# Kernel tuning notes

Measured on AMD Instinct MI355X. Metric: run time of the kernel, lower is better.

## Reference

```python
import jax, jax.numpy as jnp
import numpy as np

DEGREE = 4
NUM_CHARTS = 8
N = 16384
IN_DIM = 29  # 3*(2*4+1) + 2 procedural params


def positional_encoding(x, degree=DEGREE):
    # Faithful to torch order: [x, sin(2^1 pi x), cos(2^1 pi x), ..., sin(2^d pi x), cos(2^d pi x)]
    pe = [x]
    for d in range(1, degree + 1):
        s = (2.0 ** d) * np.pi
        pe.append(jnp.sin(s * x))
        pe.append(jnp.cos(s * x))
    return jnp.concatenate(pe, axis=-1)


def setup_inputs() -> dict:
    key = jax.random.key(0)
    ks = jax.random.split(key, 9)
    h = 256
    sc = 0.05
    return {
        "x": jax.random.normal(ks[0], (N, 3), jnp.float32),
        "proc": jax.random.normal(ks[1], (1, 2), jnp.float32),
        "W0": jax.random.normal(ks[2], (NUM_CHARTS, IN_DIM, h), jnp.float32) * sc,
        "b0": jax.random.normal(ks[3], (NUM_CHARTS, h), jnp.float32) * sc,
        "Wh": jax.random.normal(ks[4], (NUM_CHARTS, 6, h, h), jnp.float32) * sc,
        "bh": jax.random.normal(ks[5], (NUM_CHARTS, 6, h), jnp.float32) * sc,
        "Wl": jax.random.normal(ks[6], (NUM_CHARTS, h, 2), jnp.float32) * sc,
        "bl": jax.random.normal(ks[7], (NUM_CHARTS, 2), jnp.float32) * sc,
        "mlp_idx": jax.random.randint(ks[8], (N,), 0, NUM_CHARTS, jnp.int32),
    }


def reference(x, proc, W0, b0, Wh, bh, Wl, bl, mlp_idx):
    xp = positional_encoding(x)                      # (N, 27)
    proc_rep = jnp.broadcast_to(proc, (xp.shape[0], proc.shape[1]))
    xp = jnp.concatenate([xp, proc_rep], axis=-1)    # (N, 29)

    out = jnp.zeros((xp.shape[0], Wl.shape[-1]), xp.dtype)
    n_hidden = Wh.shape[1]
    for c in range(NUM_CHARTS):                      # small fixed chart loop
        h = jax.nn.relu(xp @ W0[c] + b0[c])          # (N, 256)
        for l in range(n_hidden):
            h = jax.nn.relu(h @ Wh[c, l] + bh[c, l])
        oc = jax.nn.sigmoid(h @ Wl[c] + bl[c])       # (N, 2)
        out = jnp.where((mlp_idx == c)[:, None], oc, out)
    return out
```

## Files before the change

kernel.cpp:

```cpp
#include <hip/hip_runtime.h>
#include <hip/hip_bf16.h>
#include <math.h>

#define NPTS   16384
#define NCH    8
#define MT     32
#define LSTR   264
#define SEG    16384
#define PSEG   2048

typedef short bf16x8 __attribute__((ext_vector_type(8)));
typedef float f32x4  __attribute__((ext_vector_type(4)));

__device__ __forceinline__ float bf2f(unsigned short u){
  union { unsigned int i; float f; } v; v.i = ((unsigned int)u) << 16; return v.f;
}
__device__ __forceinline__ unsigned short f2bf(float f){
  union { float f; unsigned int i; } v; v.f = f;
  unsigned int x = v.i;
  return (unsigned short)((x + 0x7fffu + ((x >> 16) & 1u)) >> 16);
}


__global__ __launch_bounds__(256) void prep_k(
    const float* __restrict__ Wh, const float* __restrict__ W0,
    const int* __restrict__ midx,
    unsigned short* __restrict__ Wth, unsigned short* __restrict__ Wt0,
    int* __restrict__ segcnt, int* __restrict__ bucket){
  int bid = blockIdx.x, tid = threadIdx.x;
  if (bid < 192){
    __shared__ __align__(16) unsigned short tile[64 * LSTR];
    int mat = bid >> 2, ck = bid & 3;
    const float* src = Wh + (size_t)mat * 65536 + (size_t)ck * 64 * 256;
    int r = tid >> 2, seg = (tid & 3) * 64;
    const float* sp = &src[r * 256 + seg];
    #pragma unroll
    for (int j8 = 0; j8 < 8; j8++){
      float4 f0 = *(const float4*)&sp[j8 * 8];
      float4 f1 = *(const float4*)&sp[j8 * 8 + 4];
      __align__(16) unsigned short t8[8];
      t8[0]=f2bf(f0.x); t8[1]=f2bf(f0.y); t8[2]=f2bf(f0.z); t8[3]=f2bf(f0.w);
      t8[4]=f2bf(f1.x); t8[5]=f2bf(f1.y); t8[6]=f2bf(f1.z); t8[7]=f2bf(f1.w);
      *(uint4*)&tile[r * LSTR + seg + j8 * 8] = *(const uint4*)t8;
    }
    __syncthreads();
    unsigned short* dst = Wth + (size_t)mat * 65536 + (size_t)ck * 16384;
    #pragma unroll
    for (int it = 0; it < 8; it++){
      int s = it * 256 + tid;
      int k8l = s >> 8, n = s & 255;
      __align__(16) unsigned short t8[8];
      #pragma unroll
      for (int j = 0; j < 8; j++) t8[j] = tile[(k8l * 8 + j) * LSTR + n];
      *(uint4*)&dst[(size_t)s * 8] = *(const uint4*)t8;
    }
  } else if (bid < 200){
    int c = bid - 192;
    #pragma unroll
    for (int it = 0; it < 4; it++){
      int s = it * 256 + tid;
      int k8 = s >> 8, n = s & 255;
      __align__(16) unsigned short t8[8];
      #pragma unroll
      for (int j = 0; j < 8; j++){
        int k = k8 * 8 + j;
        t8[j] = (k < 29) ? f2bf(W0[(c * 29 + k) * 256 + n]) : (unsigned short)0;
      }
      *(uint4*)&Wt0[(size_t)c * 8192 + (size_t)s * 8] = *(const uint4*)t8;
    }
  } else {
    __shared__ int cur[NCH];
    int sb = bid - 200;
    int lane = tid & 63;
    if (tid < NCH) cur[tid] = 0;
    __syncthreads();
    for (int it = 0; it < 8; it++){
      int i = sb * PSEG + it * 256 + tid;
      int c = midx[i];
      #pragma unroll
      for (int cc = 0; cc < NCH; cc++){
        unsigned long long m = __ballot(c == cc);
        if (!m) continue;
        int leader = (int)(__ffsll((long long)m) - 1);
        int wb = 0;
        if (lane == leader) wb = atomicAdd(&cur[cc], (int)__popcll(m));
        wb = __shfl(wb, leader);
        if (c == cc){
          int rk = (int)__popcll(m & ((1ull << lane) - 1));
          bucket[cc * SEG + sb * PSEG + wb + rk] = i;
        }
      }
    }
    __syncthreads();
    if (tid < NCH) segcnt[sb * NCH + tid] = cur[tid];
  }
}


#define LOADG(g) do {                                                          \
    const unsigned short* _p = wlane + (size_t)(g) * 8192;                     \
    asm volatile("global_load_dwordx4 %0, %4, off\n\t"                         \
                 "global_load_dwordx4 %1, %4, off offset:256\n\t"              \
                 "global_load_dwordx4 %2, %4, off offset:512\n\t"              \
                 "global_load_dwordx4 %3, %4, off offset:768"                  \
        : "=&v"(br[g][0]), "=&v"(br[g][1]), "=&v"(br[g][2]), "=&v"(br[g][3])   \
        : "v"(_p));                                                            \
  } while (0)

#define WAITG(g, n)                                                            \
  asm volatile("s_waitcnt vmcnt(" #n ")"                                       \
      : "+v"(br[g][0]), "+v"(br[g][1]), "+v"(br[g][2]), "+v"(br[g][3]))

#define MFMAG(g)                                                               \
  {                                                                            \
    bf16x8 a0 = *(const bf16x8*)&ain[(l15) * LSTR + (g) * 32 + quad * 8];      \
    bf16x8 a1 = *(const bf16x8*)&ain[(16 + l15) * LSTR + (g) * 32 + quad * 8]; \
    _Pragma("unroll")                                                          \
    for (int nt = 0; nt < 4; nt++){                                            \
      acc[0][nt] = __builtin_amdgcn_mfma_f32_16x16x32_bf16(                    \
          a0, br[g][nt], ((g) == 0) ? zz : acc[0][nt], 0, 0, 0);               \
      acc[1][nt] = __builtin_amdgcn_mfma_f32_16x16x32_bf16(                    \
          a1, br[g][nt], ((g) == 0) ? zz : acc[1][nt], 0, 0, 0);               \
    }                                                                          \
  }

__global__ __launch_bounds__(256) void mlp_k(
    const float* __restrict__ x,
    const float* __restrict__ proc,
    const float* __restrict__ b0,
    const float* __restrict__ bh,
    const float* __restrict__ Wl,
    const float* __restrict__ bl,
    const unsigned short* __restrict__ Wt0,
    const unsigned short* __restrict__ Wth,
    const int* __restrict__ segcnt,
    const int* __restrict__ bucket,
    float* __restrict__ out)
{
  __shared__ __align__(16) unsigned short actA[MT * LSTR];
  __shared__ __align__(16) unsigned short actB[MT * LSTR];
  __shared__ unsigned short biasb[7 * 256];
  __shared__ unsigned short wlb[512];
  __shared__ int ridx[MT];

  int chart = blockIdx.x & 7;
  int tile  = blockIdx.x >> 3;

  int pre[9];
  pre[0] = 0;
  #pragma unroll
  for (int s = 0; s < 8; s++) pre[s + 1] = pre[s] + segcnt[s * NCH + chart];
  int total = pre[8];
  int cnt = total - tile * MT;
  if (cnt <= 0) return;
  if (cnt > MT) cnt = MT;

  int tid  = threadIdx.x;
  int lane = tid & 63;
  int wv   = tid >> 6;
  int l15  = lane & 15;
  int quad = lane >> 4;
  int cb   = wv * 64;

  biasb[tid] = f2bf(b0[chart * 256 + tid]);
  #pragma unroll
  for (int j = 0; j < 6; j++)
    biasb[(j + 1) * 256 + tid] = f2bf(bh[(chart * 6 + j) * 256 + tid]);
  wlb[tid]       = f2bf(Wl[chart * 512 + tid]);
  wlb[256 + tid] = f2bf(Wl[chart * 512 + 256 + tid]);

  if (tid < MT){
    int row = tid;
    int g = -1;
    if (row < cnt){
      int r = tile * MT + row;
      int sb = 0, off = 0;
      #pragma unroll
      for (int s = 0; s < 8; s++)
        if (r >= pre[s]){ sb = s; off = r - pre[s]; }
      g = bucket[chart * SEG + sb * PSEG + off];
    }
    ridx[row] = g;
    unsigned short* rowp = &actA[row * LSTR];
    if (g >= 0){
      float xv0 = x[g*3+0], xv1 = x[g*3+1], xv2 = x[g*3+2];
      rowp[0] = f2bf(xv0); rowp[1] = f2bf(xv1); rowp[2] = f2bf(xv2);
      #pragma unroll
      for (int d = 1; d <= 4; d++){
        float s = (float)(1 << d) * 3.14159265358979323846f;
        int o = 3 + (d - 1) * 6;
        rowp[o+0] = f2bf(sinf(s*xv0)); rowp[o+1] = f2bf(sinf(s*xv1)); rowp[o+2] = f2bf(sinf(s*xv2));
        rowp[o+3] = f2bf(cosf(s*xv0)); rowp[o+4] = f2bf(cosf(s*xv1)); rowp[o+5] = f2bf(cosf(s*xv2));
      }
      rowp[27] = f2bf(proc[0]); rowp[28] = f2bf(proc[1]);
      rowp[29] = 0; rowp[30] = 0; rowp[31] = 0;
    } else {
      #pragma unroll
      for (int k = 0; k < 32; k++) rowp[k] = 0;
    }
  }
  __syncthreads();

  f32x4 acc[2][4];
  const f32x4 zz = {0.f, 0.f, 0.f, 0.f};

  {
    const unsigned short* W0p = Wt0 + chart * 8192;
    bf16x8 b0r[4];
    #pragma unroll
    for (int nt = 0; nt < 4; nt++)
      b0r[nt] = *(const bf16x8*)&W0p[(size_t)(quad * 256 + cb + nt * 16 + l15) * 8];
    #pragma unroll
    for (int mt = 0; mt < 2; mt++){
      bf16x8 a0 = *(const bf16x8*)&actA[(mt * 16 + l15) * LSTR + quad * 8];
      #pragma unroll
      for (int nt = 0; nt < 4; nt++)
        acc[mt][nt] = __builtin_amdgcn_mfma_f32_16x16x32_bf16(a0, b0r[nt], zz, 0, 0, 0);
    }
    #pragma unroll
    for (int nt = 0; nt < 4; nt++){
      int col = cb + nt * 16 + l15;
      float bias = bf2f(biasb[col]);
      #pragma unroll
      for (int mt = 0; mt < 2; mt++)
        #pragma unroll
        for (int r = 0; r < 4; r++){
          float v = acc[mt][nt][r] + bias;
          v = v > 0.f ? v : 0.f;
          actB[(mt * 16 + quad * 4 + r) * LSTR + col] = f2bf(v);
        }
    }
  }
  __syncthreads();

  for (int l = 1; l <= 6; l++){
    const unsigned short* wlane = Wth + ((size_t)(chart * 6 + l - 1) << 16)
                                + (size_t)(quad * 256 + cb + l15) * 8;
    const unsigned short* ain = (l & 1) ? actB : actA;
    unsigned short* aout      = (l & 1) ? actA : actB;

    bf16x8 br[8][4];
    LOADG(0); LOADG(1); LOADG(2); LOADG(3);
    LOADG(4); LOADG(5); LOADG(6); LOADG(7);

    WAITG(0, 28); MFMAG(0);
    WAITG(1, 24); MFMAG(1);
    WAITG(2, 20); MFMAG(2);
    WAITG(3, 16); MFMAG(3);
    WAITG(4, 12); MFMAG(4);
    WAITG(5, 8);  MFMAG(5);
    WAITG(6, 4);  MFMAG(6);
    WAITG(7, 0);  MFMAG(7);

    #pragma unroll
    for (int nt = 0; nt < 4; nt++){
      int col = cb + nt * 16 + l15;
      float bias = bf2f(biasb[l * 256 + col]);
      #pragma unroll
      for (int mt = 0; mt < 2; mt++)
        #pragma unroll
        for (int r = 0; r < 4; r++){
          float v = acc[mt][nt][r] + bias;
          v = v > 0.f ? v : 0.f;
          aout[(mt * 16 + quad * 4 + r) * LSTR + col] = f2bf(v);
        }
    }
    __syncthreads();
  }

  {
    int m = tid >> 3;
    int p = tid & 7;
    const unsigned short* hrow = actB + m * LSTR + p * 32;
    const unsigned short* wlp = wlb + p * 64;
    float s0 = 0.f, s1 = 0.f;
    #pragma unroll 8
    for (int k = 0; k < 32; k += 2){
      unsigned int w01 = *(const unsigned int*)&wlp[k * 2];
      unsigned int w23 = *(const unsigned int*)&wlp[k * 2 + 2];
      unsigned int h2  = *(const unsigned int*)&hrow[k];
      float hv0 = bf2f((unsigned short)(h2 & 0xffff));
      float hv1 = bf2f((unsigned short)(h2 >> 16));
      s0 += hv0 * bf2f((unsigned short)(w01 & 0xffff)) + hv1 * bf2f((unsigned short)(w23 & 0xffff));
      s1 += hv0 * bf2f((unsigned short)(w01 >> 16))    + hv1 * bf2f((unsigned short)(w23 >> 16));
    }
    s0 += __shfl_xor(s0, 1); s0 += __shfl_xor(s0, 2); s0 += __shfl_xor(s0, 4);
    s1 += __shfl_xor(s1, 1); s1 += __shfl_xor(s1, 2); s1 += __shfl_xor(s1, 4);
    if (p == 0){
      int g = ridx[m];
      if (g >= 0){
        float o0 = 1.f / (1.f + __expf(-(s0 + bl[chart*2+0])));
        float o1 = 1.f / (1.f + __expf(-(s1 + bl[chart*2+1])));
        *(float2*)&out[(size_t)g * 2] = make_float2(o0, o1);
      }
    }
  }
}


extern "C" void kernel_launch(void* const* d_in, const int* in_sizes, int n_in,
                              void* d_out, int out_size, void* d_ws, size_t ws_size,
                              hipStream_t stream){
  const float* x    = (const float*)d_in[0];
  const float* proc = (const float*)d_in[1];
  const float* W0   = (const float*)d_in[2];
  const float* b0   = (const float*)d_in[3];
  const float* Wh   = (const float*)d_in[4];
  const float* bh   = (const float*)d_in[5];
  const float* Wl   = (const float*)d_in[6];
  const float* bl   = (const float*)d_in[7];
  const int* midx = (const int*)d_in[8];
  float* out = (float*)d_out;

  char* ws = (char*)d_ws;
  int* segcnt = (int*)ws;
  int* bucket = segcnt + 64;
  size_t off = (((size_t)(64 + NCH * SEG)) * 4 + 15) & ~(size_t)15;
  unsigned short* Wt0 = (unsigned short*)(ws + off);
  unsigned short* Wth = Wt0 + NCH * 8192;

  hipLaunchKernelGGL(prep_k, dim3(208),  dim3(256), 0, stream,
                     Wh, W0, midx, Wth, Wt0, segcnt, bucket);
  hipLaunchKernelGGL(mlp_k,  dim3(4096), dim3(256), 0, stream,
                     x, proc, b0, bh, Wl, bl, Wt0, Wth, segcnt, bucket, out);
}
```

Baseline: 128.6 us.

## Double MLP row tile to 64 and software-pipeline weight loads with four slots

```diff
diff --git a/kernel.cpp b/kernel.cpp
--- a/kernel.cpp
+++ b/kernel.cpp
@@ -4,7 +4,7 @@
 
 #define NPTS   16384
 #define NCH    8
-#define MT     32
+#define MT     64
 #define LSTR   264
 #define SEG    16384
 #define PSEG   2048
@@ -97,34 +97,35 @@
 }
 
 
-#define LOADG(g) do {                                                          \
+#define LOADG(slot, g) do {                                                    \
     const unsigned short* _p = wlane + (size_t)(g) * 8192;                     \
     asm volatile("global_load_dwordx4 %0, %4, off\n\t"                         \
                  "global_load_dwordx4 %1, %4, off offset:256\n\t"              \
                  "global_load_dwordx4 %2, %4, off offset:512\n\t"              \
                  "global_load_dwordx4 %3, %4, off offset:768"                  \
-        : "=&v"(br[g][0]), "=&v"(br[g][1]), "=&v"(br[g][2]), "=&v"(br[g][3])   \
+        : "=&v"(br[slot][0]), "=&v"(br[slot][1]),                              \
+          "=&v"(br[slot][2]), "=&v"(br[slot][3])                               \
         : "v"(_p));                                                            \
   } while (0)
 
-#define WAITG(g, n)                                                            \
+#define WAITG(slot, n)                                                         \
   asm volatile("s_waitcnt vmcnt(" #n ")"                                       \
-      : "+v"(br[g][0]), "+v"(br[g][1]), "+v"(br[g][2]), "+v"(br[g][3]))
-
-#define MFMAG(g)                                                               \
+      : "+v"(br[slot][0]), "+v"(br[slot][1]),                                  \
+        "+v"(br[slot][2]), "+v"(br[slot][3]))
+
+#define MFMAG(slot, g)                                                         \
   {                                                                            \
-    bf16x8 a0 = *(const bf16x8*)&ain[(l15) * LSTR + (g) * 32 + quad * 8];      \
-    bf16x8 a1 = *(const bf16x8*)&ain[(16 + l15) * LSTR + (g) * 32 + quad * 8]; \
     _Pragma("unroll")                                                          \
-    for (int nt = 0; nt < 4; nt++){                                            \
-      acc[0][nt] = __builtin_amdgcn_mfma_f32_16x16x32_bf16(                    \
-          a0, br[g][nt], ((g) == 0) ? zz : acc[0][nt], 0, 0, 0);               \
-      acc[1][nt] = __builtin_amdgcn_mfma_f32_16x16x32_bf16(                    \
-          a1, br[g][nt], ((g) == 0) ? zz : acc[1][nt], 0, 0, 0);               \
+    for (int mt = 0; mt < 4; mt++){                                            \
+      bf16x8 a = *(const bf16x8*)&ain[(mt * 16 + l15) * LSTR + (g) * 32 + quad * 8]; \
+      _Pragma("unroll")                                                        \
+      for (int nt = 0; nt < 4; nt++)                                           \
+        acc[mt][nt] = __builtin_amdgcn_mfma_f32_16x16x32_bf16(                 \
+            a, br[slot][nt], ((g) == 0) ? zz : acc[mt][nt], 0, 0, 0);          \
     }                                                                          \
   }
 
-__global__ __launch_bounds__(256) void mlp_k(
+__global__ __launch_bounds__(256, 1) void mlp_k(
     const float* __restrict__ x,
     const float* __restrict__ proc,
     const float* __restrict__ b0,
@@ -201,7 +202,7 @@
   }
   __syncthreads();
 
-  f32x4 acc[2][4];
+  f32x4 acc[4][4];
   const f32x4 zz = {0.f, 0.f, 0.f, 0.f};
 
   {
@@ -211,7 +212,7 @@
     for (int nt = 0; nt < 4; nt++)
       b0r[nt] = *(const bf16x8*)&W0p[(size_t)(quad * 256 + cb + nt * 16 + l15) * 8];
     #pragma unroll
-    for (int mt = 0; mt < 2; mt++){
+    for (int mt = 0; mt < 4; mt++){
       bf16x8 a0 = *(const bf16x8*)&actA[(mt * 16 + l15) * LSTR + quad * 8];
       #pragma unroll
       for (int nt = 0; nt < 4; nt++)
@@ -222,7 +223,7 @@
       int col = cb + nt * 16 + l15;
       float bias = bf2f(biasb[col]);
       #pragma unroll
-      for (int mt = 0; mt < 2; mt++)
+      for (int mt = 0; mt < 4; mt++)
         #pragma unroll
         for (int r = 0; r < 4; r++){
           float v = acc[mt][nt][r] + bias;
@@ -239,25 +240,24 @@
     const unsigned short* ain = (l & 1) ? actB : actA;
     unsigned short* aout      = (l & 1) ? actA : actB;
 
-    bf16x8 br[8][4];
-    LOADG(0); LOADG(1); LOADG(2); LOADG(3);
-    LOADG(4); LOADG(5); LOADG(6); LOADG(7);
-
-    WAITG(0, 28); MFMAG(0);
-    WAITG(1, 24); MFMAG(1);
-    WAITG(2, 20); MFMAG(2);
-    WAITG(3, 16); MFMAG(3);
-    WAITG(4, 12); MFMAG(4);
-    WAITG(5, 8);  MFMAG(5);
-    WAITG(6, 4);  MFMAG(6);
-    WAITG(7, 0);  MFMAG(7);
+    bf16x8 br[4][4];
+    LOADG(0, 0); LOADG(1, 1); LOADG(2, 2); LOADG(3, 3);
+
+    WAITG(0, 12); MFMAG(0, 0); LOADG(0, 4);
+    WAITG(1, 12); MFMAG(1, 1); LOADG(1, 5);
+    WAITG(2, 12); MFMAG(2, 2); LOADG(2, 6);
+    WAITG(3, 12); MFMAG(3, 3); LOADG(3, 7);
+    WAITG(0, 12); MFMAG(0, 4);
+    WAITG(1, 8);  MFMAG(1, 5);
+    WAITG(2, 4);  MFMAG(2, 6);
+    WAITG(3, 0);  MFMAG(3, 7);
 
     #pragma unroll
     for (int nt = 0; nt < 4; nt++){
       int col = cb + nt * 16 + l15;
       float bias = bf2f(biasb[l * 256 + col]);
       #pragma unroll
-      for (int mt = 0; mt < 2; mt++)
+      for (int mt = 0; mt < 4; mt++)
         #pragma unroll
         for (int r = 0; r < 4; r++){
           float v = acc[mt][nt][r] + bias;
@@ -269,13 +269,13 @@
   }
 
   {
-    int m = tid >> 3;
-    int p = tid & 7;
-    const unsigned short* hrow = actB + m * LSTR + p * 32;
-    const unsigned short* wlp = wlb + p * 64;
+    int m = tid >> 2;
+    int p = tid & 3;
+    const unsigned short* hrow = actB + m * LSTR + p * 64;
+    const unsigned short* wlp = wlb + p * 128;
     float s0 = 0.f, s1 = 0.f;
     #pragma unroll 8
-    for (int k = 0; k < 32; k += 2){
+    for (int k = 0; k < 64; k += 2){
       unsigned int w01 = *(const unsigned int*)&wlp[k * 2];
       unsigned int w23 = *(const unsigned int*)&wlp[k * 2 + 2];
       unsigned int h2  = *(const unsigned int*)&hrow[k];
@@ -284,8 +284,8 @@
       s0 += hv0 * bf2f((unsigned short)(w01 & 0xffff)) + hv1 * bf2f((unsigned short)(w23 & 0xffff));
       s1 += hv0 * bf2f((unsigned short)(w01 >> 16))    + hv1 * bf2f((unsigned short)(w23 >> 16));
     }
-    s0 += __shfl_xor(s0, 1); s0 += __shfl_xor(s0, 2); s0 += __shfl_xor(s0, 4);
-    s1 += __shfl_xor(s1, 1); s1 += __shfl_xor(s1, 2); s1 += __shfl_xor(s1, 4);
+    s0 += __shfl_xor(s0, 1); s0 += __shfl_xor(s0, 2);
+    s1 += __shfl_xor(s1, 1); s1 += __shfl_xor(s1, 2);
     if (p == 0){
       int g = ridx[m];
       if (g >= 0){
@@ -321,6 +321,6 @@
 
   hipLaunchKernelGGL(prep_k, dim3(208),  dim3(256), 0, stream,
                      Wh, W0, midx, Wth, Wt0, segcnt, bucket);
-  hipLaunchKernelGGL(mlp_k,  dim3(4096), dim3(256), 0, stream,
+  hipLaunchKernelGGL(mlp_k,  dim3(2048), dim3(256), 0, stream,
                      x, proc, b0, bh, Wl, bl, Wt0, Wth, segcnt, bucket, out);
 }
```

New measurement: 120.5 us. 6.3% less time.
